# Kernel tuning notes

Measured on AMD Instinct MI355X. Metric: run time of the kernel, lower is better.

## Reference

```python
import jax, jax.numpy as jnp
import numpy as np

N_NODES = 100000
N_EDGES = 1600000
N_FEAT = 128
HIDDEN = 64


def gcn_conv(x, W, b, src, dst, ew, n_nodes):
    """Faithful PyG GCNConv with edge_weight and default add_self_loops=True.

    out[i] = sum_{(j->i) in E} norm_ji * (x_j @ W^T) + d_i^{-1} * (x_i @ W^T) + b
    where deg_i = 1 + sum of incoming edge weights (self-loop weight 1),
    norm_ji = deg_j^{-1/2} * ew_ji * deg_i^{-1/2}.
    """
    xw = x @ W.T  # [N, H] -- transform first (PyG applies lin before propagate)
    deg = jnp.ones((n_nodes,), x.dtype) + jax.ops.segment_sum(ew, dst, num_segments=n_nodes)
    dis = jnp.where(deg > 0, jax.lax.rsqrt(deg), 0.0)  # deg^{-1/2}
    norm = dis[src] * ew * dis[dst]  # [E]
    msgs = norm[:, None] * xw[src]  # [E, H] gathered messages
    agg = jax.ops.segment_sum(msgs, dst, num_segments=n_nodes)  # scatter-add at targets
    agg = agg + (dis * dis)[:, None] * xw  # self-loop contribution (weight 1)
    return agg + b


def setup_inputs() -> dict:
    key = jax.random.key(0)
    k1, k2, k3, k4, k5, k6, k7, k8 = jax.random.split(key, 8)
    x = jax.random.normal(k1, (N_NODES, N_FEAT), dtype=jnp.float32)
    edge_index = jax.random.randint(k2, (2, N_EDGES), 0, N_NODES, dtype=jnp.int64)
    edge_attr = jax.random.uniform(k3, (N_EDGES,), dtype=jnp.float32)
    batch = jnp.zeros((N_NODES,), dtype=jnp.int64)
    s1 = 1.0 / np.sqrt(N_FEAT)
    s2 = 1.0 / np.sqrt(HIDDEN)
    W1 = jax.random.uniform(k4, (HIDDEN, N_FEAT), jnp.float32, -s1, s1)
    b1 = jnp.zeros((HIDDEN,), jnp.float32)
    W2 = jax.random.uniform(k5, (HIDDEN, HIDDEN), jnp.float32, -s2, s2)
    b2 = jnp.zeros((HIDDEN,), jnp.float32)
    W3 = jax.random.uniform(k6, (1, HIDDEN), jnp.float32, -s2, s2)
    b3 = jax.random.uniform(k7, (1,), jnp.float32, -s2, s2)
    return {"x": x, "edge_index": edge_index, "edge_attr": edge_attr, "batch": batch,
            "W1": W1, "b1": b1, "W2": W2, "b2": b2, "W3": W3, "b3": b3}


def reference(x, edge_index, edge_attr, batch, W1, b1, W2, b2, W3, b3):
    src, dst = edge_index[0], edge_index[1]
    n = x.shape[0]
    h = jax.nn.relu(gcn_conv(x, W1, b1, src, dst, edge_attr, n))
    h = jax.nn.relu(gcn_conv(h, W2, b2, src, dst, edge_attr, n))
    return h @ W3.T + b3  # [N, 1]
```

## Files before the change

### kernel.cpp

```cpp
#include <hip/hip_runtime.h>
#include <hip/hip_fp16.h>

#define NFEAT 128
#define HID 64
#define CAP 64


__device__ __forceinline__ float4 ld_h4(const uint2* __restrict__ p, size_t idx) {
    uint2 u = p[idx];
    __half2 a = *reinterpret_cast<const __half2*>(&u.x);
    __half2 b = *reinterpret_cast<const __half2*>(&u.y);
    float2 fa = __half22float2(a);
    float2 fb = __half22float2(b);
    return make_float4(fa.x, fa.y, fb.x, fb.y);
}


template <int K, bool HALF_OUT>
__device__ __forceinline__ void xw_body(const float* __restrict__ x,
                                        const float* __restrict__ W,
                                        void* __restrict__ outv, int M,
                                        int bidx, int tid) {
    int lane = tid & 63;
    int cg = __builtin_amdgcn_readfirstlane(tid >> 6);
    int row = bidx * 64 + lane;
    if (row >= M) return;

    const float4* xr = (const float4*)(x + (size_t)row * K);
    const float4* Wr = (const float4*)(W + (size_t)cg * 16 * K);

    float acc[16];
#pragma unroll
    for (int h = 0; h < 16; ++h) acc[h] = 0.0f;

#pragma unroll 4
    for (int kc = 0; kc < K / 4; ++kc) {
        float4 xv = xr[kc];
#pragma unroll
        for (int h = 0; h < 16; ++h) {
            float4 wv = Wr[h * (K / 4) + kc];
            acc[h] = fmaf(xv.x, wv.x, acc[h]);
            acc[h] = fmaf(xv.y, wv.y, acc[h]);
            acc[h] = fmaf(xv.z, wv.z, acc[h]);
            acc[h] = fmaf(xv.w, wv.w, acc[h]);
        }
    }

    if (HALF_OUT) {
        __half2 hp[8];
#pragma unroll
        for (int j = 0; j < 8; ++j)
            hp[j] = __float22half2_rn(make_float2(acc[2 * j], acc[2 * j + 1]));
        uint4 u0 = make_uint4(*(unsigned*)&hp[0], *(unsigned*)&hp[1],
                              *(unsigned*)&hp[2], *(unsigned*)&hp[3]);
        uint4 u1 = make_uint4(*(unsigned*)&hp[4], *(unsigned*)&hp[5],
                              *(unsigned*)&hp[6], *(unsigned*)&hp[7]);
        uint4* o = (uint4*)((char*)outv + (size_t)row * 128 + cg * 32);
        o[0] = u0;
        o[1] = u1;
    } else {
        float* out = (float*)outv;
        float4* o = (float4*)(out + (size_t)row * HID + cg * 16);
#pragma unroll
        for (int q = 0; q < 4; ++q)
            o[q] = make_float4(acc[4 * q], acc[4 * q + 1], acc[4 * q + 2], acc[4 * q + 3]);
    }
}


__global__ __launch_bounds__(256) void k_fill_xw1(const int* __restrict__ src,
                                                  const int* __restrict__ dst,
                                                  const float* __restrict__ ew,
                                                  int* cnt, unsigned* __restrict__ csr,
                                                  const float* __restrict__ x,
                                                  const float* __restrict__ W1,
                                                  void* __restrict__ xwout,
                                                  int ne, int gXW, int M) {
    int b = blockIdx.x;
    if (b < gXW) {
        xw_body<NFEAT, true>(x, W1, xwout, M, b, threadIdx.x);
    } else {
        int e = (b - gXW) * 256 + threadIdx.x;
        if (e < ne) {
            int d = dst[e];
            unsigned qq = __float2uint_rn(ew[e] * 32767.0f);
            int slot = atomicAdd(&cnt[d], 1);
            if (slot < CAP)
                csr[((size_t)d << 6) + slot] = ((unsigned)src[e] & 0x1FFFFu) | (qq << 17);
        }
    }
}


__global__ __launch_bounds__(256) void k_deg(const int* __restrict__ cnt,
                                             const unsigned* __restrict__ csr,
                                             float* __restrict__ dis, int n) {
    int i = blockIdx.x * 256 + threadIdx.x;
    if (i >= n) return;
    int c = min(cnt[i], CAP);
    const uint4* row = (const uint4*)(csr + ((size_t)i << 6));
    float s = 0.0f;
    int rounds = (c + 3) >> 2;
    for (int r = 0; r < rounds; ++r) {
        uint4 u = row[r];
        int b = r * 4;
        s += (b + 0 < c) ? (float)(u.x >> 17) : 0.0f;
        s += (b + 1 < c) ? (float)(u.y >> 17) : 0.0f;
        s += (b + 2 < c) ? (float)(u.z >> 17) : 0.0f;
        s += (b + 3 < c) ? (float)(u.w >> 17) : 0.0f;
    }
    dis[i] = rsqrtf(1.0f + s * (1.0f / 32767.0f));
}


__global__ __launch_bounds__(256) void k_xw2(const uint2* __restrict__ xh,
                                             const float* __restrict__ W,
                                             uint2* __restrict__ out, int M) {
    int lane = threadIdx.x & 63;
    int cg = __builtin_amdgcn_readfirstlane(threadIdx.x >> 6);
    int row = blockIdx.x * 64 + lane;
    if (row >= M) return;

    const uint2* xr = xh + (size_t)row * 16;
    const float4* Wr = (const float4*)(W + (size_t)cg * 16 * HID);

    float acc[16];
#pragma unroll
    for (int h = 0; h < 16; ++h) acc[h] = 0.0f;

#pragma unroll 4
    for (int kc = 0; kc < 16; ++kc) {
        float4 xv = ld_h4(xr, kc);
#pragma unroll
        for (int h = 0; h < 16; ++h) {
            float4 wv = Wr[h * 16 + kc];
            acc[h] = fmaf(xv.x, wv.x, acc[h]);
            acc[h] = fmaf(xv.y, wv.y, acc[h]);
            acc[h] = fmaf(xv.z, wv.z, acc[h]);
            acc[h] = fmaf(xv.w, wv.w, acc[h]);
        }
    }

    __half2 hp[8];
#pragma unroll
    for (int j = 0; j < 8; ++j)
        hp[j] = __float22half2_rn(make_float2(acc[2 * j], acc[2 * j + 1]));
    uint4 u0 = make_uint4(*(unsigned*)&hp[0], *(unsigned*)&hp[1],
                          *(unsigned*)&hp[2], *(unsigned*)&hp[3]);
    uint4 u1 = make_uint4(*(unsigned*)&hp[4], *(unsigned*)&hp[5],
                          *(unsigned*)&hp[6], *(unsigned*)&hp[7]);
    uint4* o = (uint4*)((char*)out + (size_t)row * 128 + cg * 32);
    o[0] = u0;
    o[1] = u1;
}


__device__ __forceinline__ float4 gather_node_h(const uint2* __restrict__ xwh,
                                                const float* __restrict__ dis,
                                                const int* __restrict__ cnt,
                                                const unsigned* __restrict__ csr,
                                                int i, int fq) {
    float di = dis[i];
    float4 sv = ld_h4(xwh, (size_t)i * 16 + fq);
    float s = di * di;
    float4 acc = make_float4(s * sv.x, s * sv.y, s * sv.z, s * sv.w);

    int c = min(cnt[i], CAP);
    const uint4* row = (const uint4*)(csr + ((size_t)i << 6));
    int rounds = (c + 3) >> 2;
    const float inv = 1.0f / 32767.0f;
    for (int r = 0; r < rounds; ++r) {
        uint4 u = row[r];
        int b = r * 4;
        unsigned s0 = u.x & 0x1FFFFu, s1 = u.y & 0x1FFFFu;
        unsigned s2 = u.z & 0x1FFFFu, s3 = u.w & 0x1FFFFu;
        float n0 = (b + 0 < c) ? dis[s0] * ((float)(u.x >> 17) * inv) * di : 0.0f;
        float n1 = (b + 1 < c) ? dis[s1] * ((float)(u.y >> 17) * inv) * di : 0.0f;
        float n2 = (b + 2 < c) ? dis[s2] * ((float)(u.z >> 17) * inv) * di : 0.0f;
        float n3 = (b + 3 < c) ? dis[s3] * ((float)(u.w >> 17) * inv) * di : 0.0f;
        float4 v0 = ld_h4(xwh, (size_t)s0 * 16 + fq);
        float4 v1 = ld_h4(xwh, (size_t)s1 * 16 + fq);
        float4 v2 = ld_h4(xwh, (size_t)s2 * 16 + fq);
        float4 v3 = ld_h4(xwh, (size_t)s3 * 16 + fq);
        acc.x = fmaf(n0, v0.x, acc.x);
        acc.y = fmaf(n0, v0.y, acc.y);
        acc.z = fmaf(n0, v0.z, acc.z);
        acc.w = fmaf(n0, v0.w, acc.w);
        acc.x = fmaf(n1, v1.x, acc.x);
        acc.y = fmaf(n1, v1.y, acc.y);
        acc.z = fmaf(n1, v1.z, acc.z);
        acc.w = fmaf(n1, v1.w, acc.w);
        acc.x = fmaf(n2, v2.x, acc.x);
        acc.y = fmaf(n2, v2.y, acc.y);
        acc.z = fmaf(n2, v2.z, acc.z);
        acc.w = fmaf(n2, v2.w, acc.w);
        acc.x = fmaf(n3, v3.x, acc.x);
        acc.y = fmaf(n3, v3.y, acc.y);
        acc.z = fmaf(n3, v3.z, acc.z);
        acc.w = fmaf(n3, v3.w, acc.w);
    }
    return acc;
}


__global__ __launch_bounds__(256) void k_gather1(const uint2* __restrict__ xwh,
                                                 const float* __restrict__ dis,
                                                 const int* __restrict__ cnt,
                                                 const unsigned* __restrict__ csr,
                                                 const float* __restrict__ b1,
                                                 uint2* __restrict__ out, int n) {
    int lane = threadIdx.x & 63;
    int g    = lane >> 4;
    int fq   = lane & 15;
    int wid   = (blockIdx.x * 256 + threadIdx.x) >> 6;
    int nwave = (gridDim.x * 256) >> 6;
    float4 bq = ((const float4*)b1)[fq];

    for (int i0 = wid * 4; i0 < n; i0 += nwave * 4) {
        int i = i0 + g;
        if (i >= n) continue;
        float4 acc = gather_node_h(xwh, dis, cnt, csr, i, fq);
        __half2 lo = __float22half2_rn(make_float2(fmaxf(acc.x + bq.x, 0.0f),
                                                   fmaxf(acc.y + bq.y, 0.0f)));
        __half2 hi = __float22half2_rn(make_float2(fmaxf(acc.z + bq.z, 0.0f),
                                                   fmaxf(acc.w + bq.w, 0.0f)));
        out[(size_t)i * 16 + fq] = make_uint2(*(unsigned*)&lo, *(unsigned*)&hi);
    }
}


__global__ __launch_bounds__(256) void k_gather2(const uint2* __restrict__ xwh,
                                                 const float* __restrict__ dis,
                                                 const int* __restrict__ cnt,
                                                 const unsigned* __restrict__ csr,
                                                 const float* __restrict__ b2,
                                                 const float* __restrict__ W3,
                                                 const float* __restrict__ b3,
                                                 float* __restrict__ out, int n) {
    int lane = threadIdx.x & 63;
    int g    = lane >> 4;
    int fq   = lane & 15;
    int wid   = (blockIdx.x * 256 + threadIdx.x) >> 6;
    int nwave = (gridDim.x * 256) >> 6;
    float4 bq = ((const float4*)b2)[fq];
    float4 wq = ((const float4*)W3)[fq];
    float bb3 = b3[0];

    for (int i0 = wid * 4; i0 < n; i0 += nwave * 4) {
        int i = i0 + g;
        if (i >= n) continue;
        float4 acc = gather_node_h(xwh, dis, cnt, csr, i, fq);
        float p = fmaxf(acc.x + bq.x, 0.0f) * wq.x
                + fmaxf(acc.y + bq.y, 0.0f) * wq.y
                + fmaxf(acc.z + bq.z, 0.0f) * wq.z
                + fmaxf(acc.w + bq.w, 0.0f) * wq.w;
        p += __shfl_xor(p, 1, 64);
        p += __shfl_xor(p, 2, 64);
        p += __shfl_xor(p, 4, 64);
        p += __shfl_xor(p, 8, 64);
        if (fq == 0) out[i] = p + bb3;
    }
}


__global__ __launch_bounds__(256) void k_xw_f32(const float* __restrict__ x,
                                                const float* __restrict__ W,
                                                float* __restrict__ out, int M, int K_is_128) {
    if (K_is_128)
        xw_body<NFEAT, false>(x, W, out, M, blockIdx.x, threadIdx.x);
    else
        xw_body<HID, false>(x, W, out, M, blockIdx.x, threadIdx.x);
}

__global__ __launch_bounds__(256) void k_deg_init1(float* deg, int n) {
    int i = blockIdx.x * 256 + threadIdx.x;
    if (i < n) deg[i] = 1.0f;
}

__global__ __launch_bounds__(256) void k_deg_accum(const int* __restrict__ dst,
                                                   const float* __restrict__ ew,
                                                   float* deg, int ne) {
    int e = blockIdx.x * 256 + threadIdx.x;
    if (e < ne) atomicAdd(&deg[dst[e]], ew[e]);
}

__global__ __launch_bounds__(256) void k_rsqrt(float* deg, int n) {
    int i = blockIdx.x * 256 + threadIdx.x;
    if (i < n) deg[i] = rsqrtf(deg[i]);
}

__global__ __launch_bounds__(256) void k_selfinit(const float* __restrict__ xw,
                                                  const float* __restrict__ dis,
                                                  float* __restrict__ agg, int n) {
    int idx = blockIdx.x * 256 + threadIdx.x;
    if (idx < n * 16) {
        int i = idx >> 4;
        float d = dis[i];
        float s = d * d;
        float4 v = ((const float4*)xw)[idx];
        ((float4*)agg)[idx] = make_float4(s * v.x, s * v.y, s * v.z, s * v.w);
    }
}

__global__ __launch_bounds__(256) void k_scatter(const int* __restrict__ src,
                                                 const int* __restrict__ dst,
                                                 const float* __restrict__ ew,
                                                 const float* __restrict__ dis,
                                                 const float* __restrict__ xw,
                                                 float* __restrict__ agg, int ne) {
    int t = threadIdx.x;
    int e = blockIdx.x * 4 + (t >> 6);
    if (e >= ne) return;
    int s = src[e], d = dst[e];
    float nrm = dis[s] * ew[e] * dis[d];
    int h = t & 63;
    atomicAdd(&agg[(size_t)d * HID + h], nrm * xw[(size_t)s * HID + h]);
}

__global__ __launch_bounds__(256) void k_bias_relu(float* __restrict__ agg,
                                                   const float* __restrict__ b, int n) {
    int idx = blockIdx.x * 256 + threadIdx.x;
    if (idx < n * 16) {
        int hq = idx & 15;
        float4 v = ((float4*)agg)[idx];
        float4 bb = ((const float4*)b)[hq];
        v.x = fmaxf(v.x + bb.x, 0.0f);
        v.y = fmaxf(v.y + bb.y, 0.0f);
        v.z = fmaxf(v.z + bb.z, 0.0f);
        v.w = fmaxf(v.w + bb.w, 0.0f);
        ((float4*)agg)[idx] = v;
    }
}

__global__ __launch_bounds__(256) void k_final(const float* __restrict__ agg,
                                               const float* __restrict__ b2,
                                               const float* __restrict__ W3,
                                               const float* __restrict__ b3,
                                               float* __restrict__ out, int n) {
    int t = threadIdx.x;
    int i = blockIdx.x * 4 + (t >> 6);
    if (i >= n) return;
    int h = t & 63;
    float v = fmaxf(agg[(size_t)i * HID + h] + b2[h], 0.0f) * W3[h];
#pragma unroll
    for (int off = 32; off > 0; off >>= 1) v += __shfl_down(v, off, 64);
    if (h == 0) out[i] = v + b3[0];
}


extern "C" void kernel_launch(void* const* d_in, const int* in_sizes, int n_in,
                              void* d_out, int out_size, void* d_ws, size_t ws_size,
                              hipStream_t stream) {
    const float* x  = (const float*)d_in[0];
    const int*   ei = (const int*)d_in[1];
    const float* ew = (const float*)d_in[2];
    const float* W1 = (const float*)d_in[4];
    const float* b1 = (const float*)d_in[5];
    const float* W2 = (const float*)d_in[6];
    const float* b2 = (const float*)d_in[7];
    const float* W3 = (const float*)d_in[8];
    const float* b3 = (const float*)d_in[9];
    float* out = (float*)d_out;

    int N = in_sizes[0] / NFEAT;
    int E = in_sizes[1] / 2;
    const int* src = ei;
    const int* dst = ei + E;

    dim3 blk(256);
    int gN  = (N + 255) / 256;
    int gE  = (E + 255) / 256;
    int gXW = (N + 63) / 64;

    size_t offA   = 0;
    size_t offB   = offA + (size_t)N * HID * 2;
    size_t offDis = offB + (size_t)N * HID * 2;
    size_t offCnt = offDis + (size_t)N * 4;
    size_t offCSR = offCnt + (size_t)N * 4;
    size_t need   = offCSR + (size_t)N * CAP * 4;

    char* ws = (char*)d_ws;

    if (ws_size >= need) {
        void*     bufA = (void*)(ws + offA);
        uint2*    bufB = (uint2*)(ws + offB);
        float*    dis  = (float*)(ws + offDis);
        int*      cnt  = (int*)(ws + offCnt);
        unsigned* csr  = (unsigned*)(ws + offCSR);

        hipMemsetAsync(cnt, 0, (size_t)N * 4, stream);
        k_fill_xw1<<<gXW + gE, blk, 0, stream>>>(src, dst, ew, cnt, csr,
                                                 x, W1, bufA, E, gXW, N);
        k_deg<<<gN, blk, 0, stream>>>(cnt, csr, dis, N);
        k_gather1<<<2048, blk, 0, stream>>>((const uint2*)bufA, dis, cnt, csr,
                                            b1, bufB, N);
        k_xw2<<<gXW, blk, 0, stream>>>((const uint2*)bufB, W2, (uint2*)bufA, N);
        k_gather2<<<2048, blk, 0, stream>>>((const uint2*)bufA, dis, cnt, csr,
                                            b2, W3, b3, out, N);
    } else {
        size_t foffA   = 0;
        size_t foffB   = foffA + (size_t)N * HID * 4;
        size_t foffDis = foffB + (size_t)N * HID * 4;
        float* bufA = (float*)(ws + foffA);
        float* bufB = (float*)(ws + foffB);
        float* dis  = (float*)(ws + foffDis);

        int gNH4 = (N * 16 + 255) / 256;
        int gE4  = (E + 3) / 4;
        int gN4  = (N + 3) / 4;
        k_deg_init1<<<gN, blk, 0, stream>>>(dis, N);
        k_deg_accum<<<gE, blk, 0, stream>>>(dst, ew, dis, E);
        k_rsqrt<<<gN, blk, 0, stream>>>(dis, N);

        k_xw_f32<<<gXW, blk, 0, stream>>>(x, W1, bufA, N, 1);
        k_selfinit<<<gNH4, blk, 0, stream>>>(bufA, dis, bufB, N);
        k_scatter<<<gE4, blk, 0, stream>>>(src, dst, ew, dis, bufA, bufB, E);
        k_bias_relu<<<gNH4, blk, 0, stream>>>(bufB, b1, N);

        k_xw_f32<<<gXW, blk, 0, stream>>>(bufB, W2, bufA, N, 0);
        k_selfinit<<<gNH4, blk, 0, stream>>>(bufA, dis, bufB, N);
        k_scatter<<<gE4, blk, 0, stream>>>(src, dst, ew, dis, bufA, bufB, E);
        k_final<<<gN4, blk, 0, stream>>>(bufB, b2, W3, b3, out, N);
    }
}
```

Measured before the change: 276.3 us.

## Prescale XW rows by deg^-1/2 to drop per-edge dis gathers

Folds the source-side deg^-1/2 factor into the transformed features: a new deg kernel rescales layer-1 XW rows in place, and k_xw2 multiplies its output by dis before storing. The gather loop then uses only the quantized edge weight, with no random dis[src] lookup per edge, and applies the destination factor once at the end. It also reorders the fused fill kernel so some XW blocks run before and others after the edge-scatter blocks, and software-prefetches the next CSR chunk. The cost is an extra read-modify-write pass over the fp16 XW buffer and one more fp16 rounding step.

```diff
diff --git a/kernel.cpp b/kernel.cpp
--- a/kernel.cpp
+++ b/kernel.cpp
@@ -13,6 +13,12 @@
     float2 fa = __half22float2(a);
     float2 fb = __half22float2(b);
     return make_float4(fa.x, fa.y, fb.x, fb.y);
+}
+
+__device__ __forceinline__ uint2 pack_h4(float a, float b, float c, float d) {
+    __half2 lo = __float22half2_rn(make_float2(a, b));
+    __half2 hi = __float22half2_rn(make_float2(c, d));
+    return make_uint2(*(unsigned*)&lo, *(unsigned*)&hi);
 }
 
 
@@ -47,17 +53,13 @@
     }
 
     if (HALF_OUT) {
-        __half2 hp[8];
-#pragma unroll
-        for (int j = 0; j < 8; ++j)
-            hp[j] = __float22half2_rn(make_float2(acc[2 * j], acc[2 * j + 1]));
-        uint4 u0 = make_uint4(*(unsigned*)&hp[0], *(unsigned*)&hp[1],
-                              *(unsigned*)&hp[2], *(unsigned*)&hp[3]);
-        uint4 u1 = make_uint4(*(unsigned*)&hp[4], *(unsigned*)&hp[5],
-                              *(unsigned*)&hp[6], *(unsigned*)&hp[7]);
+        uint2 hp[4];
+#pragma unroll
+        for (int j = 0; j < 4; ++j)
+            hp[j] = pack_h4(acc[4 * j], acc[4 * j + 1], acc[4 * j + 2], acc[4 * j + 3]);
         uint4* o = (uint4*)((char*)outv + (size_t)row * 128 + cg * 32);
-        o[0] = u0;
-        o[1] = u1;
+        o[0] = make_uint4(hp[0].x, hp[0].y, hp[1].x, hp[1].y);
+        o[1] = make_uint4(hp[2].x, hp[2].y, hp[3].x, hp[3].y);
     } else {
         float* out = (float*)outv;
         float4* o = (float4*)(out + (size_t)row * HID + cg * 16);
@@ -75,12 +77,13 @@
                                                   const float* __restrict__ x,
                                                   const float* __restrict__ W1,
                                                   void* __restrict__ xwout,
-                                                  int ne, int gXW, int M) {
+                                                  int ne, int gXW, int gE, int M) {
     int b = blockIdx.x;
-    if (b < gXW) {
+    int PRE = gXW < 256 ? gXW : 256;
+    if (b < PRE) {
         xw_body<NFEAT, true>(x, W1, xwout, M, b, threadIdx.x);
-    } else {
-        int e = (b - gXW) * 256 + threadIdx.x;
+    } else if (b < PRE + gE) {
+        int e = (b - PRE) * 256 + threadIdx.x;
         if (e < ne) {
             int d = dst[e];
             unsigned qq = __float2uint_rn(ew[e] * 32767.0f);
@@ -88,33 +91,49 @@
             if (slot < CAP)
                 csr[((size_t)d << 6) + slot] = ((unsigned)src[e] & 0x1FFFFu) | (qq << 17);
         }
-    }
-}
-
-
-__global__ __launch_bounds__(256) void k_deg(const int* __restrict__ cnt,
-                                             const unsigned* __restrict__ csr,
-                                             float* __restrict__ dis, int n) {
-    int i = blockIdx.x * 256 + threadIdx.x;
-    if (i >= n) return;
-    int c = min(cnt[i], CAP);
-    const uint4* row = (const uint4*)(csr + ((size_t)i << 6));
-    float s = 0.0f;
-    int rounds = (c + 3) >> 2;
-    for (int r = 0; r < rounds; ++r) {
-        uint4 u = row[r];
-        int b = r * 4;
-        s += (b + 0 < c) ? (float)(u.x >> 17) : 0.0f;
-        s += (b + 1 < c) ? (float)(u.y >> 17) : 0.0f;
-        s += (b + 2 < c) ? (float)(u.z >> 17) : 0.0f;
-        s += (b + 3 < c) ? (float)(u.w >> 17) : 0.0f;
-    }
-    dis[i] = rsqrtf(1.0f + s * (1.0f / 32767.0f));
+    } else {
+        xw_body<NFEAT, true>(x, W1, xwout, M, b - gE, threadIdx.x);
+    }
+}
+
+
+__global__ __launch_bounds__(256) void k_deg_scale(const int* __restrict__ cnt,
+                                                   const unsigned* __restrict__ csr,
+                                                   float* __restrict__ dis,
+                                                   uint2* __restrict__ xwh, int n) {
+    int lane = threadIdx.x & 63;
+    int g    = lane >> 4;
+    int fq   = lane & 15;
+    int wid   = (blockIdx.x * 256 + threadIdx.x) >> 6;
+    int nwave = (gridDim.x * 256) >> 6;
+
+    for (int i0 = wid * 4; i0 < n; i0 += nwave * 4) {
+        int i = i0 + g;
+        if (i >= n) continue;
+        int c = min(cnt[i], CAP);
+        const uint4* row = (const uint4*)(csr + ((size_t)i << 6));
+        float s = 0.0f;
+        int rounds = (c + 3) >> 2;
+        for (int r = 0; r < rounds; ++r) {
+            uint4 u = row[r];
+            int b = r * 4;
+            s += (b + 0 < c) ? (float)(u.x >> 17) : 0.0f;
+            s += (b + 1 < c) ? (float)(u.y >> 17) : 0.0f;
+            s += (b + 2 < c) ? (float)(u.z >> 17) : 0.0f;
+            s += (b + 3 < c) ? (float)(u.w >> 17) : 0.0f;
+        }
+        float di = rsqrtf(1.0f + s * (1.0f / 32767.0f));
+        if (fq == 0) dis[i] = di;
+        size_t idx = (size_t)i * 16 + fq;
+        float4 v = ld_h4(xwh, idx);
+        xwh[idx] = pack_h4(di * v.x, di * v.y, di * v.z, di * v.w);
+    }
 }
 
 
 __global__ __launch_bounds__(256) void k_xw2(const uint2* __restrict__ xh,
                                              const float* __restrict__ W,
+                                             const float* __restrict__ dis,
                                              uint2* __restrict__ out, int M) {
     int lane = threadIdx.x & 63;
     int cg = __builtin_amdgcn_readfirstlane(threadIdx.x >> 6);
@@ -141,69 +160,73 @@
         }
     }
 
-    __half2 hp[8];
-#pragma unroll
-    for (int j = 0; j < 8; ++j)
-        hp[j] = __float22half2_rn(make_float2(acc[2 * j], acc[2 * j + 1]));
-    uint4 u0 = make_uint4(*(unsigned*)&hp[0], *(unsigned*)&hp[1],
-                          *(unsigned*)&hp[2], *(unsigned*)&hp[3]);
-    uint4 u1 = make_uint4(*(unsigned*)&hp[4], *(unsigned*)&hp[5],
-                          *(unsigned*)&hp[6], *(unsigned*)&hp[7]);
+    float di = dis[row];
+    uint2 hp[4];
+#pragma unroll
+    for (int j = 0; j < 4; ++j)
+        hp[j] = pack_h4(di * acc[4 * j], di * acc[4 * j + 1],
+                        di * acc[4 * j + 2], di * acc[4 * j + 3]);
     uint4* o = (uint4*)((char*)out + (size_t)row * 128 + cg * 32);
-    o[0] = u0;
-    o[1] = u1;
-}
-
-
-__device__ __forceinline__ float4 gather_node_h(const uint2* __restrict__ xwh,
+    o[0] = make_uint4(hp[0].x, hp[0].y, hp[1].x, hp[1].y);
+    o[1] = make_uint4(hp[2].x, hp[2].y, hp[3].x, hp[3].y);
+}
+
+
+__device__ __forceinline__ float4 gather_node_h(const uint2* __restrict__ T,
                                                 const float* __restrict__ dis,
                                                 const int* __restrict__ cnt,
                                                 const unsigned* __restrict__ csr,
                                                 int i, int fq) {
     float di = dis[i];
-    float4 sv = ld_h4(xwh, (size_t)i * 16 + fq);
-    float s = di * di;
-    float4 acc = make_float4(s * sv.x, s * sv.y, s * sv.z, s * sv.w);
+    float4 tself = ld_h4(T, (size_t)i * 16 + fq);
+    float4 acc = make_float4(0.f, 0.f, 0.f, 0.f);
 
     int c = min(cnt[i], CAP);
     const uint4* row = (const uint4*)(csr + ((size_t)i << 6));
     int rounds = (c + 3) >> 2;
     const float inv = 1.0f / 32767.0f;
+
+    uint4 u = (rounds > 0) ? row[0] : make_uint4(0, 0, 0, 0);
     for (int r = 0; r < rounds; ++r) {
-        uint4 u = row[r];
+        uint4 nx = (r + 1 < rounds) ? row[r + 1] : u;
         int b = r * 4;
         unsigned s0 = u.x & 0x1FFFFu, s1 = u.y & 0x1FFFFu;
         unsigned s2 = u.z & 0x1FFFFu, s3 = u.w & 0x1FFFFu;
-        float n0 = (b + 0 < c) ? dis[s0] * ((float)(u.x >> 17) * inv) * di : 0.0f;
-        float n1 = (b + 1 < c) ? dis[s1] * ((float)(u.y >> 17) * inv) * di : 0.0f;
-        float n2 = (b + 2 < c) ? dis[s2] * ((float)(u.z >> 17) * inv) * di : 0.0f;
-        float n3 = (b + 3 < c) ? dis[s3] * ((float)(u.w >> 17) * inv) * di : 0.0f;
-        float4 v0 = ld_h4(xwh, (size_t)s0 * 16 + fq);
-        float4 v1 = ld_h4(xwh, (size_t)s1 * 16 + fq);
-        float4 v2 = ld_h4(xwh, (size_t)s2 * 16 + fq);
-        float4 v3 = ld_h4(xwh, (size_t)s3 * 16 + fq);
-        acc.x = fmaf(n0, v0.x, acc.x);
-        acc.y = fmaf(n0, v0.y, acc.y);
-        acc.z = fmaf(n0, v0.z, acc.z);
-        acc.w = fmaf(n0, v0.w, acc.w);
-        acc.x = fmaf(n1, v1.x, acc.x);
-        acc.y = fmaf(n1, v1.y, acc.y);
-        acc.z = fmaf(n1, v1.z, acc.z);
-        acc.w = fmaf(n1, v1.w, acc.w);
-        acc.x = fmaf(n2, v2.x, acc.x);
-        acc.y = fmaf(n2, v2.y, acc.y);
-        acc.z = fmaf(n2, v2.z, acc.z);
-        acc.w = fmaf(n2, v2.w, acc.w);
-        acc.x = fmaf(n3, v3.x, acc.x);
-        acc.y = fmaf(n3, v3.y, acc.y);
-        acc.z = fmaf(n3, v3.z, acc.z);
-        acc.w = fmaf(n3, v3.w, acc.w);
-    }
+        float w0 = (b + 0 < c) ? (float)(u.x >> 17) : 0.0f;
+        float w1 = (b + 1 < c) ? (float)(u.y >> 17) : 0.0f;
+        float w2 = (b + 2 < c) ? (float)(u.z >> 17) : 0.0f;
+        float w3 = (b + 3 < c) ? (float)(u.w >> 17) : 0.0f;
+        float4 v0 = ld_h4(T, (size_t)s0 * 16 + fq);
+        float4 v1 = ld_h4(T, (size_t)s1 * 16 + fq);
+        float4 v2 = ld_h4(T, (size_t)s2 * 16 + fq);
+        float4 v3 = ld_h4(T, (size_t)s3 * 16 + fq);
+        acc.x = fmaf(w0, v0.x, acc.x);
+        acc.y = fmaf(w0, v0.y, acc.y);
+        acc.z = fmaf(w0, v0.z, acc.z);
+        acc.w = fmaf(w0, v0.w, acc.w);
+        acc.x = fmaf(w1, v1.x, acc.x);
+        acc.y = fmaf(w1, v1.y, acc.y);
+        acc.z = fmaf(w1, v1.z, acc.z);
+        acc.w = fmaf(w1, v1.w, acc.w);
+        acc.x = fmaf(w2, v2.x, acc.x);
+        acc.y = fmaf(w2, v2.y, acc.y);
+        acc.z = fmaf(w2, v2.z, acc.z);
+        acc.w = fmaf(w2, v2.w, acc.w);
+        acc.x = fmaf(w3, v3.x, acc.x);
+        acc.y = fmaf(w3, v3.y, acc.y);
+        acc.z = fmaf(w3, v3.z, acc.z);
+        acc.w = fmaf(w3, v3.w, acc.w);
+        u = nx;
+    }
+    acc.x = di * fmaf(acc.x, inv, tself.x);
+    acc.y = di * fmaf(acc.y, inv, tself.y);
+    acc.z = di * fmaf(acc.z, inv, tself.z);
+    acc.w = di * fmaf(acc.w, inv, tself.w);
     return acc;
 }
 
 
-__global__ __launch_bounds__(256) void k_gather1(const uint2* __restrict__ xwh,
+__global__ __launch_bounds__(256) void k_gather1(const uint2* __restrict__ T,
                                                  const float* __restrict__ dis,
                                                  const int* __restrict__ cnt,
                                                  const unsigned* __restrict__ csr,
@@ -219,17 +242,16 @@
     for (int i0 = wid * 4; i0 < n; i0 += nwave * 4) {
         int i = i0 + g;
         if (i >= n) continue;
-        float4 acc = gather_node_h(xwh, dis, cnt, csr, i, fq);
-        __half2 lo = __float22half2_rn(make_float2(fmaxf(acc.x + bq.x, 0.0f),
-                                                   fmaxf(acc.y + bq.y, 0.0f)));
-        __half2 hi = __float22half2_rn(make_float2(fmaxf(acc.z + bq.z, 0.0f),
-                                                   fmaxf(acc.w + bq.w, 0.0f)));
-        out[(size_t)i * 16 + fq] = make_uint2(*(unsigned*)&lo, *(unsigned*)&hi);
-    }
-}
-
-
-__global__ __launch_bounds__(256) void k_gather2(const uint2* __restrict__ xwh,
+        float4 acc = gather_node_h(T, dis, cnt, csr, i, fq);
+        out[(size_t)i * 16 + fq] = pack_h4(fmaxf(acc.x + bq.x, 0.0f),
+                                           fmaxf(acc.y + bq.y, 0.0f),
+                                           fmaxf(acc.z + bq.z, 0.0f),
+                                           fmaxf(acc.w + bq.w, 0.0f));
+    }
+}
+
+
+__global__ __launch_bounds__(256) void k_gather2(const uint2* __restrict__ T,
                                                  const float* __restrict__ dis,
                                                  const int* __restrict__ cnt,
                                                  const unsigned* __restrict__ csr,
@@ -249,7 +271,7 @@
     for (int i0 = wid * 4; i0 < n; i0 += nwave * 4) {
         int i = i0 + g;
         if (i >= n) continue;
-        float4 acc = gather_node_h(xwh, dis, cnt, csr, i, fq);
+        float4 acc = gather_node_h(T, dis, cnt, csr, i, fq);
         float p = fmaxf(acc.x + bq.x, 0.0f) * wq.x
                 + fmaxf(acc.y + bq.y, 0.0f) * wq.y
                 + fmaxf(acc.z + bq.z, 0.0f) * wq.z
@@ -390,11 +412,11 @@
 
         hipMemsetAsync(cnt, 0, (size_t)N * 4, stream);
         k_fill_xw1<<<gXW + gE, blk, 0, stream>>>(src, dst, ew, cnt, csr,
-                                                 x, W1, bufA, E, gXW, N);
-        k_deg<<<gN, blk, 0, stream>>>(cnt, csr, dis, N);
+                                                 x, W1, bufA, E, gXW, gE, N);
+        k_deg_scale<<<2048, blk, 0, stream>>>(cnt, csr, dis, (uint2*)bufA, N);
         k_gather1<<<2048, blk, 0, stream>>>((const uint2*)bufA, dis, cnt, csr,
                                             b1, bufB, N);
-        k_xw2<<<gXW, blk, 0, stream>>>((const uint2*)bufB, W2, (uint2*)bufA, N);
+        k_xw2<<<gXW, blk, 0, stream>>>((const uint2*)bufB, W2, dis, (uint2*)bufA, N);
         k_gather2<<<2048, blk, 0, stream>>>((const uint2*)bufA, dis, cnt, csr,
                                             b2, W3, b3, out, N);
     } else {
```

Result: slower. 311.9 us (+12.9%).

## Pack edge count and quantized weight sum into one 64-bit atomic

Applied to the files above, without the earlier changes.

The fill kernel now does a single 64-bit atomicAdd that carries both the slot counter (upper bits) and the running sum of quantized edge weights (lower 40 bits). The degree kernel no longer rereads each node's CSR row; it only decodes the packed word into a clamped count and the inverse square-root degree. The gather loop also prefetches the next CSR quad before processing the current one. The cost is a wider atomic on every edge and an extra 8 bytes per node of workspace, plus the fp16 packing is routed through a shared helper.

```diff
diff --git a/kernel.cpp b/kernel.cpp
--- a/kernel.cpp
+++ b/kernel.cpp
@@ -13,6 +13,12 @@
     float2 fa = __half22float2(a);
     float2 fb = __half22float2(b);
     return make_float4(fa.x, fa.y, fb.x, fb.y);
+}
+
+__device__ __forceinline__ uint2 pack_h4(float a, float b, float c, float d) {
+    __half2 lo = __float22half2_rn(make_float2(a, b));
+    __half2 hi = __float22half2_rn(make_float2(c, d));
+    return make_uint2(*(unsigned*)&lo, *(unsigned*)&hi);
 }
 
 
@@ -47,17 +53,13 @@
     }
 
     if (HALF_OUT) {
-        __half2 hp[8];
-#pragma unroll
-        for (int j = 0; j < 8; ++j)
-            hp[j] = __float22half2_rn(make_float2(acc[2 * j], acc[2 * j + 1]));
-        uint4 u0 = make_uint4(*(unsigned*)&hp[0], *(unsigned*)&hp[1],
-                              *(unsigned*)&hp[2], *(unsigned*)&hp[3]);
-        uint4 u1 = make_uint4(*(unsigned*)&hp[4], *(unsigned*)&hp[5],
-                              *(unsigned*)&hp[6], *(unsigned*)&hp[7]);
+        uint2 hp[4];
+#pragma unroll
+        for (int j = 0; j < 4; ++j)
+            hp[j] = pack_h4(acc[4 * j], acc[4 * j + 1], acc[4 * j + 2], acc[4 * j + 3]);
         uint4* o = (uint4*)((char*)outv + (size_t)row * 128 + cg * 32);
-        o[0] = u0;
-        o[1] = u1;
+        o[0] = make_uint4(hp[0].x, hp[0].y, hp[1].x, hp[1].y);
+        o[1] = make_uint4(hp[2].x, hp[2].y, hp[3].x, hp[3].y);
     } else {
         float* out = (float*)outv;
         float4* o = (float4*)(out + (size_t)row * HID + cg * 16);
@@ -71,7 +73,8 @@
 __global__ __launch_bounds__(256) void k_fill_xw1(const int* __restrict__ src,
                                                   const int* __restrict__ dst,
                                                   const float* __restrict__ ew,
-                                                  int* cnt, unsigned* __restrict__ csr,
+                                                  unsigned long long* pack,
+                                                  unsigned* __restrict__ csr,
                                                   const float* __restrict__ x,
                                                   const float* __restrict__ W1,
                                                   void* __restrict__ xwout,
@@ -84,7 +87,9 @@
         if (e < ne) {
             int d = dst[e];
             unsigned qq = __float2uint_rn(ew[e] * 32767.0f);
-            int slot = atomicAdd(&cnt[d], 1);
+            unsigned long long old =
+                atomicAdd(&pack[d], (1ULL << 40) | (unsigned long long)qq);
+            int slot = (int)(old >> 40);
             if (slot < CAP)
                 csr[((size_t)d << 6) + slot] = ((unsigned)src[e] & 0x1FFFFu) | (qq << 17);
         }
@@ -92,24 +97,15 @@
 }
 
 
-__global__ __launch_bounds__(256) void k_deg(const int* __restrict__ cnt,
-                                             const unsigned* __restrict__ csr,
-                                             float* __restrict__ dis, int n) {
+__global__ __launch_bounds__(256) void k_dis(const unsigned long long* __restrict__ pack,
+                                             float* __restrict__ dis,
+                                             int* __restrict__ cnt, int n) {
     int i = blockIdx.x * 256 + threadIdx.x;
     if (i >= n) return;
-    int c = min(cnt[i], CAP);
-    const uint4* row = (const uint4*)(csr + ((size_t)i << 6));
-    float s = 0.0f;
-    int rounds = (c + 3) >> 2;
-    for (int r = 0; r < rounds; ++r) {
-        uint4 u = row[r];
-        int b = r * 4;
-        s += (b + 0 < c) ? (float)(u.x >> 17) : 0.0f;
-        s += (b + 1 < c) ? (float)(u.y >> 17) : 0.0f;
-        s += (b + 2 < c) ? (float)(u.z >> 17) : 0.0f;
-        s += (b + 3 < c) ? (float)(u.w >> 17) : 0.0f;
-    }
-    dis[i] = rsqrtf(1.0f + s * (1.0f / 32767.0f));
+    unsigned long long p = pack[i];
+    int c = (int)(p >> 40);
+    cnt[i] = c < CAP ? c : CAP;
+    dis[i] = rsqrtf(1.0f + (float)(double)(p & 0xFFFFFFFFFFULL) * (1.0f / 32767.0f));
 }
 
 
@@ -141,17 +137,13 @@
         }
     }
 
-    __half2 hp[8];
-#pragma unroll
-    for (int j = 0; j < 8; ++j)
-        hp[j] = __float22half2_rn(make_float2(acc[2 * j], acc[2 * j + 1]));
-    uint4 u0 = make_uint4(*(unsigned*)&hp[0], *(unsigned*)&hp[1],
-                          *(unsigned*)&hp[2], *(unsigned*)&hp[3]);
-    uint4 u1 = make_uint4(*(unsigned*)&hp[4], *(unsigned*)&hp[5],
-                          *(unsigned*)&hp[6], *(unsigned*)&hp[7]);
+    uint2 hp[4];
+#pragma unroll
+    for (int j = 0; j < 4; ++j)
+        hp[j] = pack_h4(acc[4 * j], acc[4 * j + 1], acc[4 * j + 2], acc[4 * j + 3]);
     uint4* o = (uint4*)((char*)out + (size_t)row * 128 + cg * 32);
-    o[0] = u0;
-    o[1] = u1;
+    o[0] = make_uint4(hp[0].x, hp[0].y, hp[1].x, hp[1].y);
+    o[1] = make_uint4(hp[2].x, hp[2].y, hp[3].x, hp[3].y);
 }
 
 
@@ -169,8 +161,10 @@
     const uint4* row = (const uint4*)(csr + ((size_t)i << 6));
     int rounds = (c + 3) >> 2;
     const float inv = 1.0f / 32767.0f;
+
+    uint4 u = (rounds > 0) ? row[0] : make_uint4(0, 0, 0, 0);
     for (int r = 0; r < rounds; ++r) {
-        uint4 u = row[r];
+        uint4 nx = (r + 1 < rounds) ? row[r + 1] : u;
         int b = r * 4;
         unsigned s0 = u.x & 0x1FFFFu, s1 = u.y & 0x1FFFFu;
         unsigned s2 = u.z & 0x1FFFFu, s3 = u.w & 0x1FFFFu;
@@ -198,6 +192,7 @@
         acc.y = fmaf(n3, v3.y, acc.y);
         acc.z = fmaf(n3, v3.z, acc.z);
         acc.w = fmaf(n3, v3.w, acc.w);
+        u = nx;
     }
     return acc;
 }
@@ -220,11 +215,10 @@
         int i = i0 + g;
         if (i >= n) continue;
         float4 acc = gather_node_h(xwh, dis, cnt, csr, i, fq);
-        __half2 lo = __float22half2_rn(make_float2(fmaxf(acc.x + bq.x, 0.0f),
-                                                   fmaxf(acc.y + bq.y, 0.0f)));
-        __half2 hi = __float22half2_rn(make_float2(fmaxf(acc.z + bq.z, 0.0f),
-                                                   fmaxf(acc.w + bq.w, 0.0f)));
-        out[(size_t)i * 16 + fq] = make_uint2(*(unsigned*)&lo, *(unsigned*)&hi);
+        out[(size_t)i * 16 + fq] = pack_h4(fmaxf(acc.x + bq.x, 0.0f),
+                                           fmaxf(acc.y + bq.y, 0.0f),
+                                           fmaxf(acc.z + bq.z, 0.0f),
+                                           fmaxf(acc.w + bq.w, 0.0f));
     }
 }
 
@@ -372,12 +366,13 @@
     int gE  = (E + 255) / 256;
     int gXW = (N + 63) / 64;
 
-    size_t offA   = 0;
-    size_t offB   = offA + (size_t)N * HID * 2;
-    size_t offDis = offB + (size_t)N * HID * 2;
-    size_t offCnt = offDis + (size_t)N * 4;
-    size_t offCSR = offCnt + (size_t)N * 4;
-    size_t need   = offCSR + (size_t)N * CAP * 4;
+    size_t offA    = 0;
+    size_t offB    = offA + (size_t)N * HID * 2;
+    size_t offDis  = offB + (size_t)N * HID * 2;
+    size_t offCnt  = offDis + (size_t)N * 4;
+    size_t offPack = offCnt + (size_t)N * 4;
+    size_t offCSR  = offPack + (size_t)N * 8;
+    size_t need    = offCSR + (size_t)N * CAP * 4;
 
     char* ws = (char*)d_ws;
 
@@ -386,12 +381,13 @@
         uint2*    bufB = (uint2*)(ws + offB);
         float*    dis  = (float*)(ws + offDis);
         int*      cnt  = (int*)(ws + offCnt);
+        unsigned long long* pack = (unsigned long long*)(ws + offPack);
         unsigned* csr  = (unsigned*)(ws + offCSR);
 
-        hipMemsetAsync(cnt, 0, (size_t)N * 4, stream);
-        k_fill_xw1<<<gXW + gE, blk, 0, stream>>>(src, dst, ew, cnt, csr,
+        hipMemsetAsync(pack, 0, (size_t)N * 8, stream);
+        k_fill_xw1<<<gXW + gE, blk, 0, stream>>>(src, dst, ew, pack, csr,
                                                  x, W1, bufA, E, gXW, N);
-        k_deg<<<gN, blk, 0, stream>>>(cnt, csr, dis, N);
+        k_dis<<<gN, blk, 0, stream>>>(pack, dis, cnt, N);
         k_gather1<<<2048, blk, 0, stream>>>((const uint2*)bufA, dis, cnt, csr,
                                             b1, bufB, N);
         k_xw2<<<gXW, blk, 0, stream>>>((const uint2*)bufB, W2, (uint2*)bufA, N);
```

Result: slower. 302.4 us (+9.5%).
